# Kernel optimization log

Hardware: AMD Instinct MI355X
Metric: run time of the kernel (lower is better)

Reference implementation:

```python
import jax, jax.numpy as jnp
import numpy as np

TAU = 2.0      # spikingjelly LIFNode default tau
V_TH = 1.0     # default v_threshold
ALPHA = 4.0    # default surrogate.Sigmoid alpha
H, HL = 8, 2   # num_heads, local_heads

@jax.custom_vjp
def spike(u):
    # Heaviside: fire when membrane potential >= threshold (u = v - v_th)
    return (u >= 0.0).astype(u.dtype)

def _spike_fwd(u):
    return spike(u), u

def _spike_bwd(u, g):
    s = jax.nn.sigmoid(ALPHA * u)
    return (g * ALPHA * s * (1.0 - s),)

spike.defvjp(_spike_fwd, _spike_bwd)

def lif(x):
    # Multi-step LIF, decay_input=False, v_reset=0.0 (hard reset), detach_reset=True.
    # Charge: v = v - (v - 0)/tau + x ; spike when v >= v_th ; reset v -> 0 where spiked.
    decay = 1.0 - 1.0 / TAU
    def step(v, xt):
        v = v * decay + xt
        s = spike(v - V_TH)
        v = v * (1.0 - jax.lax.stop_gradient(s))  # detach_reset
        return v, s
    _, spikes = jax.lax.scan(step, jnp.zeros_like(x[0]), x)
    return spikes

def setup_inputs() -> dict:
    key = jax.random.key(0)
    ks = jax.random.split(key, 5)
    T, B, C, D = 4, 8, 512, 768
    hd = D // H            # 96
    mkv = hd * HL          # 192 (GQA kv projection width)
    scale = 0.1            # keeps LIF membrane potentials near threshold
    return {
        "x": jax.random.normal(ks[0], (T, B, C, D), jnp.float32),
        "q_w": jax.random.normal(ks[1], (D, D), jnp.float32) * scale,
        "k_w": jax.random.normal(ks[2], (mkv, D), jnp.float32) * scale,
        "v_w": jax.random.normal(ks[3], (mkv, D), jnp.float32) * scale,
        "wo_w": jax.random.normal(ks[4], (D, D), jnp.float32) * scale,
    }

def reference(x, q_w, k_w, v_w, wo_w):
    T, B, C, D = x.shape
    hd = D // H
    n_rep = H // HL
    xs = lif(x)  # proj_lif
    # q: (T,B,C,D) -> (T,B,H,C,hd)
    q = lif(xs @ q_w.T).reshape(T, B, C, H, hd).transpose(0, 1, 3, 2, 4)
    # k,v: (T,B,C,mkv) -> repeat_interleave over kv heads -> (T,B,H,C,hd)
    k = lif(xs @ k_w.T).reshape(T, B, C, HL, hd)
    k = jnp.repeat(k, n_rep, axis=3).transpose(0, 1, 3, 2, 4)
    v = lif(xs @ v_w.T).reshape(T, B, C, HL, hd)
    v = jnp.repeat(v, n_rep, axis=3).transpose(0, 1, 3, 2, 4)
    # softmax-free attention: (q k^T) * 0.1 @ v
    scores = jnp.einsum('tbhqd,tbhkd->tbhqk', q, k) * 0.1
    out = jnp.einsum('tbhqk,tbhkd->tbhqd', scores, v)
    # (T,B,H,C,hd) -> (T,B,C,D)
    out = out.transpose(0, 1, 3, 2, 4).reshape(T, B, C, D)
    return out @ wo_w.T
```

## Files before the change

kernel.cpp:

```cpp
#include <hip/hip_runtime.h>

typedef __bf16 bf16;
typedef __bf16 bf16x8 __attribute__((ext_vector_type(8)));
typedef float f32x4 __attribute__((ext_vector_type(4)));

#define T_ 4
#define B_ 8
#define C_ 512
#define D_ 768
#define H_ 8
#define HL_ 2
#define HD_ 96
#define MKV_ 192
#define M2_ 4096
#define BCD_ 3145728
#define M3_ 16384
#define NCOMB 1152
#define SUSP_CAP 65536
#define SUSP_WIN 2e-4f

__device__ __forceinline__ void gld16(const bf16* g, bf16* l) {
    __builtin_amdgcn_global_load_lds(
        (const __attribute__((address_space(1))) unsigned int*)g,
        (__attribute__((address_space(3))) unsigned int*)l, 16, 0, 0);
}

__global__ __launch_bounds__(256) void prep_kernel(
    const float* __restrict__ x, const float* __restrict__ q_w,
    const float* __restrict__ k_w, const float* __restrict__ v_w,
    const float* __restrict__ wo_w, bf16* __restrict__ xs,
    bf16* __restrict__ whi, bf16* __restrict__ wlo, bf16* __restrict__ wo_bf,
    unsigned* __restrict__ susp)
{
    const int t0 = blockIdx.x * 256 + threadIdx.x;
    const int stride = gridDim.x * 256;
    if (t0 == 0) susp[0] = 0;
    for (int i = t0; i < BCD_; i += stride) {
        double v = 0.0;
        #pragma unroll
        for (int t = 0; t < T_; ++t) {
            v = v * 0.5 + (double)x[(size_t)t * BCD_ + i];
            float s = (v >= 1.0) ? 1.0f : 0.0f;
            xs[(size_t)t * BCD_ + i] = (bf16)s;
            if (s != 0.0f) v = 0.0;
        }
    }
    for (int i = t0; i < NCOMB * D_; i += stride) {
        int row = i / D_, col = i - row * D_;
        float v;
        if (row < 768)      v = q_w[(size_t)row * D_ + col];
        else if (row < 960) v = k_w[(size_t)(row - 768) * D_ + col];
        else                v = v_w[(size_t)(row - 960) * D_ + col];
        bf16 h = (bf16)v;
        whi[i] = h;
        wlo[i] = (bf16)(v - (float)h);
    }
    for (int i = t0; i < D_ * D_; i += stride)
        wo_bf[i] = (bf16)wo_w[i];
}

__global__ __launch_bounds__(256, 3) void proj_lif_kernel(
    const bf16* __restrict__ xs, const bf16* __restrict__ Whi,
    const bf16* __restrict__ Wlo,
    bf16* __restrict__ q_sp, bf16* __restrict__ k_sp, bf16* __restrict__ v_sp,
    unsigned* __restrict__ susp)
{
    __shared__ __align__(16) bf16 A0[T_][64 * 32];
    __shared__ __align__(16) bf16 A1[T_][64 * 32];
    __shared__ __align__(16) bf16 H0[64 * 32];
    __shared__ __align__(16) bf16 H1[64 * 32];
    __shared__ __align__(16) bf16 L0[64 * 32];
    __shared__ __align__(16) bf16 L1[64 * 32];

    const int tid  = threadIdx.x;
    const int wave = tid >> 6, lane = tid & 63;
    const int m16  = lane & 15, quad = lane >> 4;
    const int wm   = wave >> 1, wn = wave & 1;

    const int bid   = blockIdx.y * 64 + blockIdx.x;
    const int xcd   = bid & 7;
    const int local = bid >> 3;
    const int m0    = ((xcd << 3) | (local & 7)) * 64;
    const int n0    = (local >> 3) * 64;

    const int colb = n0 + wn * 32;
    bf16* outp; int Nloc, cb;
    if (colb < 768)      { outp = q_sp; Nloc = 768; cb = colb; }
    else if (colb < 960) { outp = k_sp; Nloc = 192; cb = colb - 768; }
    else                 { outp = v_sp; Nloc = 192; cb = colb - 960; }

    f32x4 acc[T_][2][2];
    #pragma unroll
    for (int t = 0; t < T_; t++)
        #pragma unroll
        for (int a = 0; a < 2; a++)
            #pragma unroll
            for (int b = 0; b < 2; b++) { f32x4 z = {0.f,0.f,0.f,0.f}; acc[t][a][b] = z; }

    const int srow = tid >> 2;
    const int sseg = (tid & 3) ^ ((tid >> 3) & 3);

#define STAGE(Ab, Hb, Lb, k0) do {                                            \
    _Pragma("unroll")                                                         \
    for (int t = 0; t < T_; t++)                                              \
        gld16(xs + (size_t)(t * M2_ + m0 + srow) * D_ + (k0) + sseg * 8,      \
              &Ab[t][tid * 8]);                                               \
    gld16(Whi + (size_t)(n0 + srow) * D_ + (k0) + sseg * 8, &Hb[tid * 8]);    \
    gld16(Wlo + (size_t)(n0 + srow) * D_ + (k0) + sseg * 8, &Lb[tid * 8]);    \
} while (0)

    bf16x8 a[T_][2], bh[2], bl[2];

#define LOADREGS(Ab, Hb, Lb) do {                                             \
    _Pragma("unroll")                                                         \
    for (int mi = 0; mi < 2; mi++) {                                          \
        int row = wm * 32 + mi * 16 + m16;                                    \
        int off = row * 32 + ((quad ^ ((row >> 1) & 3)) * 8);                 \
        _Pragma("unroll")                                                     \
        for (int t = 0; t < T_; t++) a[t][mi] = *(const bf16x8*)&Ab[t][off];  \
    }                                                                         \
    _Pragma("unroll")                                                         \
    for (int ni = 0; ni < 2; ni++) {                                          \
        int row = wn * 32 + ni * 16 + m16;                                    \
        int off = row * 32 + ((quad ^ ((row >> 1) & 3)) * 8);                 \
        bh[ni] = *(const bf16x8*)&Hb[off];                                    \
        bl[ni] = *(const bf16x8*)&Lb[off];                                    \
    }                                                                         \
} while (0)

#define DOMFMA() do {                                                         \
    __builtin_amdgcn_s_setprio(1);                                            \
    _Pragma("unroll")                                                         \
    for (int ni = 0; ni < 2; ni++)                                            \
        _Pragma("unroll")                                                     \
        for (int t = 0; t < T_; t++)                                          \
            _Pragma("unroll")                                                 \
            for (int mi = 0; mi < 2; mi++) {                                  \
                acc[t][mi][ni] = __builtin_amdgcn_mfma_f32_16x16x32_bf16(     \
                    a[t][mi], bh[ni], acc[t][mi][ni], 0, 0, 0);               \
                acc[t][mi][ni] = __builtin_amdgcn_mfma_f32_16x16x32_bf16(     \
                    a[t][mi], bl[ni], acc[t][mi][ni], 0, 0, 0);               \
            }                                                                 \
    __builtin_amdgcn_s_setprio(0);                                            \
} while (0)

#define READS_DONE() do {                                                     \
    asm volatile("s_waitcnt lgkmcnt(0)" ::: "memory");                        \
    __builtin_amdgcn_s_barrier();                                             \
    __builtin_amdgcn_sched_barrier(0);                                        \
} while (0)

#define NEXT_READY(N) do {                                                    \
    asm volatile("s_waitcnt vmcnt(" #N ")" ::: "memory");                     \
    __builtin_amdgcn_s_barrier();                                             \
} while (0)

    STAGE(A0, H0, L0, 0);
    STAGE(A1, H1, L1, 32);
    NEXT_READY(6);

    for (int s = 0; s < 22; s += 2) {
        LOADREGS(A0, H0, L0);
        READS_DONE();
        STAGE(A0, H0, L0, (s + 2) * 32);
        DOMFMA();
        NEXT_READY(6);

        LOADREGS(A1, H1, L1);
        READS_DONE();
        STAGE(A1, H1, L1, (s + 3) * 32);
        DOMFMA();
        NEXT_READY(6);
    }
    LOADREGS(A0, H0, L0);
    READS_DONE();
    DOMFMA();
    NEXT_READY(0);
    LOADREGS(A1, H1, L1);
    DOMFMA();

#undef STAGE
#undef LOADREGS
#undef DOMFMA
#undef READS_DONE
#undef NEXT_READY

    #pragma unroll
    for (int mi = 0; mi < 2; mi++)
        #pragma unroll
        for (int ni = 0; ni < 2; ni++)
            #pragma unroll
            for (int rr = 0; rr < 4; rr++) {
                int row = m0 + wm * 32 + mi * 16 + quad * 4 + rr;
                int lc  = cb + ni * 16 + m16;
                float v = 0.f;
                bool suspect = false;
                #pragma unroll
                for (int t = 0; t < T_; t++) {
                    v = v * 0.5f + acc[t][mi][ni][rr];
                    float d = v - 1.0f;
                    if (fabsf(d) < SUSP_WIN) suspect = true;
                    float sp = (d >= 0.f) ? 1.f : 0.f;
                    v *= (1.f - sp);
                    outp[(size_t)(t * M2_ + row) * Nloc + lc] = (bf16)sp;
                }
                if (suspect) {
                    int ccol = n0 + wn * 32 + ni * 16 + m16;
                    unsigned idx = atomicAdd(susp, 1u);
                    if (idx < SUSP_CAP) susp[1 + idx] = (unsigned)(row * 2048 + ccol);
                }
            }
}

__global__ __launch_bounds__(256) void fixup_kernel(
    const bf16* __restrict__ xs, const float* __restrict__ q_w,
    const float* __restrict__ k_w, const float* __restrict__ v_w,
    bf16* __restrict__ q_sp, bf16* __restrict__ k_sp, bf16* __restrict__ v_sp,
    const unsigned* __restrict__ susp)
{
    unsigned count = susp[0];
    if (count > SUSP_CAP) count = SUSP_CAP;
    const int lane = threadIdx.x & 63;
    const int wid  = (blockIdx.x * blockDim.x + threadIdx.x) >> 6;
    const int nw   = (gridDim.x * blockDim.x) >> 6;
    for (unsigned i = wid; i < count; i += nw) {
        unsigned e = susp[1 + i];
        int row = e >> 11, col = e & 2047;
        const float* W; bf16* outp; int Nloc, lc;
        if (col < 768)      { W = q_w + (size_t)col * D_;         outp = q_sp; Nloc = 768; lc = col; }
        else if (col < 960) { W = k_w + (size_t)(col - 768) * D_; outp = k_sp; Nloc = 192; lc = col - 768; }
        else                { W = v_w + (size_t)(col - 960) * D_; outp = v_sp; Nloc = 192; lc = col - 960; }
        double v = 0.0;
        for (int t = 0; t < T_; ++t) {
            const bf16* ar = xs + (size_t)(t * M2_ + row) * D_;
            double y = 0.0;
            for (int k = lane; k < D_; k += 64)
                y += (double)(float)ar[k] * (double)W[k];
            #pragma unroll
            for (int off = 1; off < 64; off <<= 1)
                y += __shfl_xor(y, off);
            v = v * 0.5 + y;
            unsigned sp = (v >= 1.0) ? 1u : 0u;
            if (lane == 0) outp[(size_t)(t * M2_ + row) * Nloc + lc] = (bf16)(float)sp;
            if (sp) v = 0.0;
        }
    }
}

__global__ __launch_bounds__(256) void ktv_kernel(
    const bf16* __restrict__ k_sp, const bf16* __restrict__ v_sp,
    float* __restrict__ M_part)
{
    const int g    = blockIdx.x;
    const int cc   = blockIdx.y;
    const int kvh  = g % HL_;
    const int tb   = g / HL_;
    const int wave = threadIdx.x >> 6;
    const int lane = threadIdx.x & 63;
    const int m16  = lane & 15, quad = lane >> 4;

    __shared__ __align__(16) bf16 klds[96 * 40];
    __shared__ __align__(16) bf16 vlds[96 * 40];

    f32x4 acc[9];
    #pragma unroll
    for (int i = 0; i < 9; i++) { f32x4 z = {0.f,0.f,0.f,0.f}; acc[i] = z; }

    const bf16* kbase = k_sp + ((size_t)tb * C_ + cc * 64) * MKV_ + kvh * HD_;
    const bf16* vbase = v_sp + ((size_t)tb * C_ + cc * 64) * MKV_ + kvh * HD_;

    for (int c0 = 0; c0 < 64; c0 += 32) {
        __syncthreads();
        for (int ci = threadIdx.x; ci < 768; ci += 256) {
            int arr = ci & 1;
            int pos = ci >> 1;
            int c = pos / 12, seg = pos - c * 12;
            const bf16* src = (arr ? vbase : kbase) + (size_t)(c0 + c) * MKV_ + seg * 8;
            bf16x8 val = *(const bf16x8*)src;
            bf16* dst = arr ? vlds : klds;
            #pragma unroll
            for (int e = 0; e < 8; e++)
                dst[(seg * 8 + e) * 40 + c] = val[e];
        }
        __syncthreads();
        #pragma unroll
        for (int i = 0; i < 9; i++) {
            int tile = wave + i * 4;
            int mt = tile / 6, nt = tile % 6;
            bf16x8 a = *(const bf16x8*)(&klds[(mt * 16 + m16) * 40 + quad * 8]);
            bf16x8 b = *(const bf16x8*)(&vlds[(nt * 16 + m16) * 40 + quad * 8]);
            acc[i] = __builtin_amdgcn_mfma_f32_16x16x32_bf16(a, b, acc[i], 0, 0, 0);
        }
    }
    float* op = M_part + ((size_t)cc * 64 + g) * HD_ * HD_;
    #pragma unroll
    for (int i = 0; i < 9; i++) {
        int tile = wave + i * 4;
        int mt = tile / 6, nt = tile % 6;
        #pragma unroll
        for (int r = 0; r < 4; r++) {
            int d = mt * 16 + quad * 4 + r;
            int j = nt * 16 + m16;
            op[(size_t)j * HD_ + d] = acc[i][r];
        }
    }
}

__global__ __launch_bounds__(256) void cvtM_kernel(
    const float* __restrict__ M_part, bf16* __restrict__ M_hi,
    bf16* __restrict__ M_lo)
{
    int i = blockIdx.x * 256 + threadIdx.x;
    if (i >= 64 * HD_ * HD_) return;
    float m = 0.f;
    #pragma unroll
    for (int j = 0; j < 8; j++)
        m += M_part[i + (size_t)j * 589824];
    bf16 h = (bf16)m;
    M_hi[i] = h;
    M_lo[i] = (bf16)(m - (float)h);
}

__global__ __launch_bounds__(256) void qm_kernel(
    const bf16* __restrict__ q_sp, const bf16* __restrict__ M_hi,
    const bf16* __restrict__ M_lo, bf16* __restrict__ out_attn)
{
    const int tbh  = blockIdx.x;
    const int h    = tbh % H_;
    const int tb   = tbh / H_;
    const int g    = tb * HL_ + (h >> 2);
    const int wave = threadIdx.x >> 6;
    const int lane = threadIdx.x & 63;
    const int m16  = lane & 15, quad = lane >> 4;
    const int cw   = blockIdx.y * 128 + wave * 32;

    __shared__ __align__(16) bf16 Mh[96 * 104];
    __shared__ __align__(16) bf16 Ml[96 * 104];
    {
        const bf16* gh = M_hi + (size_t)g * HD_ * HD_;
        const bf16* gl = M_lo + (size_t)g * HD_ * HD_;
        #pragma unroll
        for (int j = 0; j < 5; j++) {
            int ci = j * 256 + threadIdx.x;
            if (ci < 1152) {
                int row = ci / 12, seg = ci % 12;
                *(bf16x8*)&Mh[row * 104 + seg * 8] = *(const bf16x8*)(gh + row * HD_ + seg * 8);
                *(bf16x8*)&Ml[row * 104 + seg * 8] = *(const bf16x8*)(gl + row * HD_ + seg * 8);
            }
        }
    }
    __syncthreads();

    f32x4 acc[2][6];
    #pragma unroll
    for (int mi = 0; mi < 2; mi++)
        #pragma unroll
        for (int nt = 0; nt < 6; nt++) { f32x4 z = {0.f,0.f,0.f,0.f}; acc[mi][nt] = z; }

    #pragma unroll
    for (int ks = 0; ks < 3; ++ks) {
        bf16x8 a[2];
        #pragma unroll
        for (int mi = 0; mi < 2; mi++)
            a[mi] = *(const bf16x8*)(q_sp + ((size_t)(tb * C_ + cw + mi * 16 + m16)) * D_
                                     + h * HD_ + ks * 32 + quad * 8);
        #pragma unroll
        for (int nt = 0; nt < 6; ++nt) {
            bf16x8 bh = *(const bf16x8*)&Mh[(nt * 16 + m16) * 104 + ks * 32 + quad * 8];
            bf16x8 bl = *(const bf16x8*)&Ml[(nt * 16 + m16) * 104 + ks * 32 + quad * 8];
            #pragma unroll
            for (int mi = 0; mi < 2; mi++) {
                acc[mi][nt] = __builtin_amdgcn_mfma_f32_16x16x32_bf16(a[mi], bh, acc[mi][nt], 0, 0, 0);
                acc[mi][nt] = __builtin_amdgcn_mfma_f32_16x16x32_bf16(a[mi], bl, acc[mi][nt], 0, 0, 0);
            }
        }
    }
    #pragma unroll
    for (int mi = 0; mi < 2; mi++)
        #pragma unroll
        for (int nt = 0; nt < 6; nt++)
            #pragma unroll
            for (int r = 0; r < 4; r++) {
                int c = cw + mi * 16 + quad * 4 + r;
                int j = nt * 16 + m16;
                out_attn[((size_t)(tb * C_ + c)) * D_ + h * HD_ + j] = (bf16)(0.1f * acc[mi][nt][r]);
            }
}

__global__ __launch_bounds__(256) void final_gemm_kernel(
    const bf16* __restrict__ A, const bf16* __restrict__ W, float* __restrict__ out)
{
    __shared__ __align__(16) bf16 Alds[128 * 64];
    __shared__ __align__(16) bf16 Blds[128 * 64];
    const int tid  = threadIdx.x;
    const int wave = tid >> 6, lane = tid & 63;
    const int m16  = lane & 15, quad = lane >> 4;
    const int wm   = wave >> 1, wn = wave & 1;
    const int m0   = blockIdx.x * 128, n0 = blockIdx.y * 128;

    f32x4 acc[4][4];
    #pragma unroll
    for (int a = 0; a < 4; a++)
        #pragma unroll
        for (int b = 0; b < 4; b++) { f32x4 z = {0.f,0.f,0.f,0.f}; acc[a][b] = z; }

    for (int k0 = 0; k0 < D_; k0 += 64) {
        __syncthreads();
        #pragma unroll
        for (int j = 0; j < 4; j++) {
            int ci = j * 256 + tid;
            int row = ci >> 3, slot = ci & 7;
            int seg = slot ^ ((row >> 1) & 7);
            gld16(A + (size_t)(m0 + row) * D_ + k0 + seg * 8, Alds + ci * 8);
            gld16(W + (size_t)(n0 + row) * D_ + k0 + seg * 8, Blds + ci * 8);
        }
        __syncthreads();
        #pragma unroll
        for (int kc = 0; kc < 2; kc++) {
            bf16x8 a[4], b[4];
            #pragma unroll
            for (int mi = 0; mi < 4; mi++) {
                int row = wm * 64 + mi * 16 + m16;
                a[mi] = *(const bf16x8*)&Alds[row * 64 + (((kc * 4 + quad) ^ ((row >> 1) & 7)) * 8)];
            }
            #pragma unroll
            for (int ni = 0; ni < 4; ni++) {
                int row = wn * 64 + ni * 16 + m16;
                b[ni] = *(const bf16x8*)&Blds[row * 64 + (((kc * 4 + quad) ^ ((row >> 1) & 7)) * 8)];
            }
            #pragma unroll
            for (int mi = 0; mi < 4; mi++)
                #pragma unroll
                for (int ni = 0; ni < 4; ni++)
                    acc[mi][ni] = __builtin_amdgcn_mfma_f32_16x16x32_bf16(a[mi], b[ni], acc[mi][ni], 0, 0, 0);
        }
    }
    #pragma unroll
    for (int mi = 0; mi < 4; mi++)
        #pragma unroll
        for (int ni = 0; ni < 4; ni++)
            #pragma unroll
            for (int r = 0; r < 4; r++) {
                int row = m0 + wm * 64 + mi * 16 + quad * 4 + r;
                int col = n0 + wn * 64 + ni * 16 + m16;
                out[(size_t)row * D_ + col] = acc[mi][ni][r];
            }
}

extern "C" void kernel_launch(void* const* d_in, const int* in_sizes, int n_in,
                              void* d_out, int out_size, void* d_ws, size_t ws_size,
                              hipStream_t stream) {
    const float* x    = (const float*)d_in[0];
    const float* q_w  = (const float*)d_in[1];
    const float* k_w  = (const float*)d_in[2];
    const float* v_w  = (const float*)d_in[3];
    const float* wo_w = (const float*)d_in[4];
    float* out = (float*)d_out;

    char* ws = (char*)d_ws;
    bf16* xs    = (bf16*)(ws);
    bf16* q_sp  = (bf16*)(ws + 25165824);
    bf16* k_sp  = (bf16*)(ws + 50331648);
    bf16* v_sp  = (bf16*)(ws + 56623104);
    bf16* whi   = (bf16*)(ws + 62914560);
    bf16* wlo   = (bf16*)(ws + 64684032);
    bf16* wo_bf = (bf16*)(ws + 66453504);
    bf16* M_hi  = (bf16*)(ws + 67633152);
    bf16* M_lo  = (bf16*)(ws + 68812800);
    unsigned* susp = (unsigned*)(ws + 69992448);
    bf16* out_attn = xs;
    float* M_part  = out;

    hipLaunchKernelGGL(prep_kernel, dim3(2048), dim3(256), 0, stream,
                       x, q_w, k_w, v_w, wo_w, xs, whi, wlo, wo_bf, susp);
    hipLaunchKernelGGL(proj_lif_kernel, dim3(M2_ / 64, NCOMB / 64), dim3(256), 0, stream,
                       xs, whi, wlo, q_sp, k_sp, v_sp, susp);
    hipLaunchKernelGGL(fixup_kernel, dim3(256), dim3(256), 0, stream,
                       xs, q_w, k_w, v_w, q_sp, k_sp, v_sp, susp);
    hipLaunchKernelGGL(ktv_kernel, dim3(T_ * B_ * HL_, 8), dim3(256), 0, stream,
                       k_sp, v_sp, M_part);
    hipLaunchKernelGGL(cvtM_kernel, dim3((64 * HD_ * HD_ + 255) / 256), dim3(256), 0, stream,
                       M_part, M_hi, M_lo);
    hipLaunchKernelGGL(qm_kernel, dim3(T_ * B_ * H_, C_ / 128), dim3(256), 0, stream,
                       q_sp, M_hi, M_lo, out_attn);
    hipLaunchKernelGGL(final_gemm_kernel, dim3(M3_ / 128, D_ / 128), dim3(256), 0, stream,
                       out_attn, wo_bf, out);
}
```

Baseline: 266.0 us.

## Switch spike projection GEMM to int8 MFMA with two-level weight quantization

Spikes are stored as int8 instead of bf16, and the combined q/k/v weights are quantized to two int8 levels (coarse plus residual) using a global max scale. The projection GEMM then uses i8 MFMA with K=64 per instruction, which halves the k-loop iterations and the bytes moved per tile. The larger quantization error is absorbed by widening the suspect window, which sends more elements to the exact fixup kernel; that kernel now adds weights selected by the spike bits instead of multiplying. The cost is an extra max-reduction pass and kernel launch plus a heavier fixup workload.

```diff
diff --git a/kernel.cpp b/kernel.cpp
--- a/kernel.cpp
+++ b/kernel.cpp
@@ -3,6 +3,8 @@
 typedef __bf16 bf16;
 typedef __bf16 bf16x8 __attribute__((ext_vector_type(8)));
 typedef float f32x4 __attribute__((ext_vector_type(4)));
+typedef int i32x4 __attribute__((ext_vector_type(4)));
+typedef signed char i8;
 
 #define T_ 4
 #define B_ 8
@@ -17,19 +19,18 @@
 #define M3_ 16384
 #define NCOMB 1152
 #define SUSP_CAP 65536
-#define SUSP_WIN 2e-4f
-
-__device__ __forceinline__ void gld16(const bf16* g, bf16* l) {
+#define SUSP_WIN 2.2e-3f
+
+__device__ __forceinline__ void gld16(const void* g, void* l) {
     __builtin_amdgcn_global_load_lds(
         (const __attribute__((address_space(1))) unsigned int*)g,
         (__attribute__((address_space(3))) unsigned int*)l, 16, 0, 0);
 }
 
-__global__ __launch_bounds__(256) void prep_kernel(
+__global__ __launch_bounds__(256) void prep_scan_kernel(
     const float* __restrict__ x, const float* __restrict__ q_w,
     const float* __restrict__ k_w, const float* __restrict__ v_w,
-    const float* __restrict__ wo_w, bf16* __restrict__ xs,
-    bf16* __restrict__ whi, bf16* __restrict__ wlo, bf16* __restrict__ wo_bf,
+    i8* __restrict__ xs, unsigned* __restrict__ wmaxb,
     unsigned* __restrict__ susp)
 {
     const int t0 = blockIdx.x * 256 + threadIdx.x;
@@ -40,37 +41,68 @@
         #pragma unroll
         for (int t = 0; t < T_; ++t) {
             v = v * 0.5 + (double)x[(size_t)t * BCD_ + i];
-            float s = (v >= 1.0) ? 1.0f : 0.0f;
-            xs[(size_t)t * BCD_ + i] = (bf16)s;
-            if (s != 0.0f) v = 0.0;
-        }
-    }
+            i8 s = (v >= 1.0) ? (i8)1 : (i8)0;
+            xs[(size_t)t * BCD_ + i] = s;
+            if (s) v = 0.0;
+        }
+    }
+    float m = 0.f;
     for (int i = t0; i < NCOMB * D_; i += stride) {
         int row = i / D_, col = i - row * D_;
         float v;
         if (row < 768)      v = q_w[(size_t)row * D_ + col];
         else if (row < 960) v = k_w[(size_t)(row - 768) * D_ + col];
         else                v = v_w[(size_t)(row - 960) * D_ + col];
-        bf16 h = (bf16)v;
-        whi[i] = h;
-        wlo[i] = (bf16)(v - (float)h);
+        m = fmaxf(m, fabsf(v));
+    }
+    #pragma unroll
+    for (int off = 1; off < 64; off <<= 1)
+        m = fmaxf(m, __shfl_xor(m, off));
+    if ((threadIdx.x & 63) == 0)
+        atomicMax(wmaxb, __float_as_uint(m));
+}
+
+__global__ __launch_bounds__(256) void prep_quant_kernel(
+    const float* __restrict__ q_w, const float* __restrict__ k_w,
+    const float* __restrict__ v_w, const float* __restrict__ wo_w,
+    const unsigned* __restrict__ wmaxb,
+    i8* __restrict__ w1, i8* __restrict__ w2, bf16* __restrict__ wo_bf)
+{
+    const float wmax = __uint_as_float(*wmaxb);
+    const float s1   = wmax * (1.0f / 127.0f);
+    const float s2   = s1 * (1.0f / 127.0f);
+    const float i1   = 1.0f / s1;
+    const float i2   = 1.0f / s2;
+    const int t0 = blockIdx.x * 256 + threadIdx.x;
+    const int stride = gridDim.x * 256;
+    for (int i = t0; i < NCOMB * D_; i += stride) {
+        int row = i / D_, col = i - row * D_;
+        float v;
+        if (row < 768)      v = q_w[(size_t)row * D_ + col];
+        else if (row < 960) v = k_w[(size_t)(row - 768) * D_ + col];
+        else                v = v_w[(size_t)(row - 960) * D_ + col];
+        float h1 = rintf(v * i1);
+        float r  = fmaf(-s1, h1, v);
+        float h2 = rintf(r * i2);
+        w1[i] = (i8)(int)h1;
+        w2[i] = (i8)(int)h2;
     }
     for (int i = t0; i < D_ * D_; i += stride)
         wo_bf[i] = (bf16)wo_w[i];
 }
 
 __global__ __launch_bounds__(256, 3) void proj_lif_kernel(
-    const bf16* __restrict__ xs, const bf16* __restrict__ Whi,
-    const bf16* __restrict__ Wlo,
+    const i8* __restrict__ xs, const i8* __restrict__ W1,
+    const i8* __restrict__ W2, const unsigned* __restrict__ wmaxb,
     bf16* __restrict__ q_sp, bf16* __restrict__ k_sp, bf16* __restrict__ v_sp,
     unsigned* __restrict__ susp)
 {
-    __shared__ __align__(16) bf16 A0[T_][64 * 32];
-    __shared__ __align__(16) bf16 A1[T_][64 * 32];
-    __shared__ __align__(16) bf16 H0[64 * 32];
-    __shared__ __align__(16) bf16 H1[64 * 32];
-    __shared__ __align__(16) bf16 L0[64 * 32];
-    __shared__ __align__(16) bf16 L1[64 * 32];
+    __shared__ __align__(16) i8 A0[T_][64 * 64];
+    __shared__ __align__(16) i8 A1[T_][64 * 64];
+    __shared__ __align__(16) i8 G0[64 * 64];
+    __shared__ __align__(16) i8 G1[64 * 64];
+    __shared__ __align__(16) i8 E0[64 * 64];
+    __shared__ __align__(16) i8 E1[64 * 64];
 
     const int tid  = threadIdx.x;
     const int wave = tid >> 6, lane = tid & 63;
@@ -89,58 +121,62 @@
     else if (colb < 960) { outp = k_sp; Nloc = 192; cb = colb - 768; }
     else                 { outp = v_sp; Nloc = 192; cb = colb - 960; }
 
-    f32x4 acc[T_][2][2];
+    const float s2 = __uint_as_float(*wmaxb) * (1.0f / (127.0f * 127.0f));
+
+    i32x4 acc[T_][2][2];
     #pragma unroll
     for (int t = 0; t < T_; t++)
         #pragma unroll
         for (int a = 0; a < 2; a++)
             #pragma unroll
-            for (int b = 0; b < 2; b++) { f32x4 z = {0.f,0.f,0.f,0.f}; acc[t][a][b] = z; }
+            for (int b = 0; b < 2; b++) { i32x4 z = {0,0,0,0}; acc[t][a][b] = z; }
 
     const int srow = tid >> 2;
     const int sseg = (tid & 3) ^ ((tid >> 3) & 3);
 
-#define STAGE(Ab, Hb, Lb, k0) do {                                            \
+#define STAGE(Ab, Gb, Eb, k0) do {                                            \
     _Pragma("unroll")                                                         \
     for (int t = 0; t < T_; t++)                                              \
-        gld16(xs + (size_t)(t * M2_ + m0 + srow) * D_ + (k0) + sseg * 8,      \
-              &Ab[t][tid * 8]);                                               \
-    gld16(Whi + (size_t)(n0 + srow) * D_ + (k0) + sseg * 8, &Hb[tid * 8]);    \
-    gld16(Wlo + (size_t)(n0 + srow) * D_ + (k0) + sseg * 8, &Lb[tid * 8]);    \
+        gld16(xs + (size_t)(t * M2_ + m0 + srow) * D_ + (k0) + sseg * 16,     \
+              &Ab[t][tid * 16]);                                              \
+    gld16(W1 + (size_t)(n0 + srow) * D_ + (k0) + sseg * 16, &Gb[tid * 16]);   \
+    gld16(W2 + (size_t)(n0 + srow) * D_ + (k0) + sseg * 16, &Eb[tid * 16]);   \
 } while (0)
 
-    bf16x8 a[T_][2], bh[2], bl[2];
-
-#define LOADREGS(Ab, Hb, Lb) do {                                             \
+    i32x4 a[T_][2], b1[2], b2[2];
+
+#define LOADREGS(Ab, Gb, Eb) do {                                             \
     _Pragma("unroll")                                                         \
     for (int mi = 0; mi < 2; mi++) {                                          \
         int row = wm * 32 + mi * 16 + m16;                                    \
-        int off = row * 32 + ((quad ^ ((row >> 1) & 3)) * 8);                 \
+        int off = row * 64 + ((quad ^ ((row >> 1) & 3)) * 16);                \
         _Pragma("unroll")                                                     \
-        for (int t = 0; t < T_; t++) a[t][mi] = *(const bf16x8*)&Ab[t][off];  \
+        for (int t = 0; t < T_; t++) a[t][mi] = *(const i32x4*)&Ab[t][off];   \
     }                                                                         \
     _Pragma("unroll")                                                         \
     for (int ni = 0; ni < 2; ni++) {                                          \
         int row = wn * 32 + ni * 16 + m16;                                    \
-        int off = row * 32 + ((quad ^ ((row >> 1) & 3)) * 8);                 \
-        bh[ni] = *(const bf16x8*)&Hb[off];                                    \
-        bl[ni] = *(const bf16x8*)&Lb[off];                                    \
+        int off = row * 64 + ((quad ^ ((row >> 1) & 3)) * 16);                \
+        b1[ni] = *(const i32x4*)&Gb[off];                                     \
+        b2[ni] = *(const i32x4*)&Eb[off];                                     \
     }                                                                         \
 } while (0)
 
 #define DOMFMA() do {                                                         \
     __builtin_amdgcn_s_setprio(1);                                            \
     _Pragma("unroll")                                                         \
-    for (int ni = 0; ni < 2; ni++)                                            \
+    for (int t = 0; t < T_; t++)                                              \
         _Pragma("unroll")                                                     \
-        for (int t = 0; t < T_; t++)                                          \
+        for (int mi = 0; mi < 2; mi++) {                                      \
+            i32x4 a127 = (a[t][mi] << 7) - a[t][mi];                          \
             _Pragma("unroll")                                                 \
-            for (int mi = 0; mi < 2; mi++) {                                  \
-                acc[t][mi][ni] = __builtin_amdgcn_mfma_f32_16x16x32_bf16(     \
-                    a[t][mi], bh[ni], acc[t][mi][ni], 0, 0, 0);               \
-                acc[t][mi][ni] = __builtin_amdgcn_mfma_f32_16x16x32_bf16(     \
-                    a[t][mi], bl[ni], acc[t][mi][ni], 0, 0, 0);               \
+            for (int ni = 0; ni < 2; ni++) {                                  \
+                acc[t][mi][ni] = __builtin_amdgcn_mfma_i32_16x16x64_i8(       \
+                    a127, b1[ni], acc[t][mi][ni], 0, 0, 0);                   \
+                acc[t][mi][ni] = __builtin_amdgcn_mfma_i32_16x16x64_i8(       \
+                    a[t][mi], b2[ni], acc[t][mi][ni], 0, 0, 0);               \
             }                                                                 \
+        }                                                                     \
     __builtin_amdgcn_s_setprio(0);                                            \
 } while (0)
 
@@ -155,28 +191,28 @@
     __builtin_amdgcn_s_barrier();                                             \
 } while (0)
 
-    STAGE(A0, H0, L0, 0);
-    STAGE(A1, H1, L1, 32);
+    STAGE(A0, G0, E0, 0);
+    STAGE(A1, G1, E1, 64);
     NEXT_READY(6);
 
-    for (int s = 0; s < 22; s += 2) {
-        LOADREGS(A0, H0, L0);
+    for (int s = 0; s < 10; s += 2) {
+        LOADREGS(A0, G0, E0);
         READS_DONE();
-        STAGE(A0, H0, L0, (s + 2) * 32);
+        STAGE(A0, G0, E0, (s + 2) * 64);
         DOMFMA();
         NEXT_READY(6);
 
-        LOADREGS(A1, H1, L1);
+        LOADREGS(A1, G1, E1);
         READS_DONE();
-        STAGE(A1, H1, L1, (s + 3) * 32);
+        STAGE(A1, G1, E1, (s + 3) * 64);
         DOMFMA();
         NEXT_READY(6);
     }
-    LOADREGS(A0, H0, L0);
+    LOADREGS(A0, G0, E0);
     READS_DONE();
     DOMFMA();
     NEXT_READY(0);
-    LOADREGS(A1, H1, L1);
+    LOADREGS(A1, G1, E1);
     DOMFMA();
 
 #undef STAGE
@@ -197,7 +233,7 @@
                 bool suspect = false;
                 #pragma unroll
                 for (int t = 0; t < T_; t++) {
-                    v = v * 0.5f + acc[t][mi][ni][rr];
+                    v = v * 0.5f + s2 * (float)acc[t][mi][ni][rr];
                     float d = v - 1.0f;
                     if (fabsf(d) < SUSP_WIN) suspect = true;
                     float sp = (d >= 0.f) ? 1.f : 0.f;
@@ -213,7 +249,7 @@
 }
 
 __global__ __launch_bounds__(256) void fixup_kernel(
-    const bf16* __restrict__ xs, const float* __restrict__ q_w,
+    const i8* __restrict__ xs, const float* __restrict__ q_w,
     const float* __restrict__ k_w, const float* __restrict__ v_w,
     bf16* __restrict__ q_sp, bf16* __restrict__ k_sp, bf16* __restrict__ v_sp,
     const unsigned* __restrict__ susp)
@@ -232,10 +268,16 @@
         else                { W = v_w + (size_t)(col - 960) * D_; outp = v_sp; Nloc = 192; lc = col - 960; }
         double v = 0.0;
         for (int t = 0; t < T_; ++t) {
-            const bf16* ar = xs + (size_t)(t * M2_ + row) * D_;
+            const i8* ar = xs + (size_t)(t * M2_ + row) * D_;
             double y = 0.0;
-            for (int k = lane; k < D_; k += 64)
-                y += (double)(float)ar[k] * (double)W[k];
+            for (int k = lane * 4; k < D_; k += 256) {
+                f32x4 wv = *(const f32x4*)(W + k);
+                unsigned ab = *(const unsigned*)(ar + k);
+                if (ab & 0x000000ffu) y += (double)wv[0];
+                if (ab & 0x0000ff00u) y += (double)wv[1];
+                if (ab & 0x00ff0000u) y += (double)wv[2];
+                if (ab & 0xff000000u) y += (double)wv[3];
+            }
             #pragma unroll
             for (int off = 1; off < 64; off <<= 1)
                 y += __shfl_xor(y, off);
@@ -458,24 +500,28 @@
     float* out = (float*)d_out;
 
     char* ws = (char*)d_ws;
-    bf16* xs    = (bf16*)(ws);
+    i8*   xs    = (i8*)(ws);
     bf16* q_sp  = (bf16*)(ws + 25165824);
     bf16* k_sp  = (bf16*)(ws + 50331648);
     bf16* v_sp  = (bf16*)(ws + 56623104);
-    bf16* whi   = (bf16*)(ws + 62914560);
-    bf16* wlo   = (bf16*)(ws + 64684032);
+    i8*   w1    = (i8*)(ws + 62914560);
+    i8*   w2    = (i8*)(ws + 63799296);
+    unsigned* wmaxb = (unsigned*)(ws + 64684032);
     bf16* wo_bf = (bf16*)(ws + 66453504);
     bf16* M_hi  = (bf16*)(ws + 67633152);
     bf16* M_lo  = (bf16*)(ws + 68812800);
     unsigned* susp = (unsigned*)(ws + 69992448);
-    bf16* out_attn = xs;
+    bf16* out_attn = (bf16*)ws;
     float* M_part  = out;
 
-    hipLaunchKernelGGL(prep_kernel, dim3(2048), dim3(256), 0, stream,
-                       x, q_w, k_w, v_w, wo_w, xs, whi, wlo, wo_bf, susp);
+    hipMemsetAsync(wmaxb, 0, 4, stream);
+    hipLaunchKernelGGL(prep_scan_kernel, dim3(2048), dim3(256), 0, stream,
+                       x, q_w, k_w, v_w, xs, wmaxb, susp);
+    hipLaunchKernelGGL(prep_quant_kernel, dim3(512), dim3(256), 0, stream,
+                       q_w, k_w, v_w, wo_w, wmaxb, w1, w2, wo_bf);
     hipLaunchKernelGGL(proj_lif_kernel, dim3(M2_ / 64, NCOMB / 64), dim3(256), 0, stream,
-                       xs, whi, wlo, q_sp, k_sp, v_sp, susp);
-    hipLaunchKernelGGL(fixup_kernel, dim3(256), dim3(256), 0, stream,
+                       xs, w1, w2, wmaxb, q_sp, k_sp, v_sp, susp);
+    hipLaunchKernelGGL(fixup_kernel, dim3(512), dim3(256), 0, stream,
                        xs, q_w, k_w, v_w, q_sp, k_sp, v_sp, susp);
     hipLaunchKernelGGL(ktv_kernel, dim3(T_ * B_ * HL_, 8), dim3(256), 0, stream,
                        k_sp, v_sp, M_part);
```

After: 519.0 us. 1.95x slower.

## Load A operand directly into registers in projection GEMM, keep only weights in LDS

Applied to the files above, without the earlier changes.

The projection+LIF kernel no longer stages the spike-input (A) tiles through shared memory. Each wave now owns 16 rows and all 64 columns, and it prefetches its A fragments for all four timesteps straight from global memory into registers, double-buffered across k-steps. Only the hi/lo weight tiles still go through LDS. This cuts LDS footprint and LDS read traffic, and the launch-bounds occupancy hint drops from 3 to 2 blocks per SM. In exchange there are uncoalesced 16-byte global loads per lane, more register pressure, and each weight fragment is now read by all four waves instead of two.

```diff
diff --git a/kernel.cpp b/kernel.cpp
--- a/kernel.cpp
+++ b/kernel.cpp
@@ -59,14 +59,12 @@
         wo_bf[i] = (bf16)wo_w[i];
 }
 
-__global__ __launch_bounds__(256, 3) void proj_lif_kernel(
+__global__ __launch_bounds__(256, 2) void proj_lif_kernel(
     const bf16* __restrict__ xs, const bf16* __restrict__ Whi,
     const bf16* __restrict__ Wlo,
     bf16* __restrict__ q_sp, bf16* __restrict__ k_sp, bf16* __restrict__ v_sp,
     unsigned* __restrict__ susp)
 {
-    __shared__ __align__(16) bf16 A0[T_][64 * 32];
-    __shared__ __align__(16) bf16 A1[T_][64 * 32];
     __shared__ __align__(16) bf16 H0[64 * 32];
     __shared__ __align__(16) bf16 H1[64 * 32];
     __shared__ __align__(16) bf16 L0[64 * 32];
@@ -75,7 +73,6 @@
     const int tid  = threadIdx.x;
     const int wave = tid >> 6, lane = tid & 63;
     const int m16  = lane & 15, quad = lane >> 4;
-    const int wm   = wave >> 1, wn = wave & 1;
 
     const int bid   = blockIdx.y * 64 + blockIdx.x;
     const int xcd   = bid & 7;
@@ -83,64 +80,56 @@
     const int m0    = ((xcd << 3) | (local & 7)) * 64;
     const int n0    = (local >> 3) * 64;
 
-    const int colb = n0 + wn * 32;
     bf16* outp; int Nloc, cb;
-    if (colb < 768)      { outp = q_sp; Nloc = 768; cb = colb; }
-    else if (colb < 960) { outp = k_sp; Nloc = 192; cb = colb - 768; }
-    else                 { outp = v_sp; Nloc = 192; cb = colb - 960; }
-
-    f32x4 acc[T_][2][2];
+    if (n0 < 768)      { outp = q_sp; Nloc = 768; cb = n0; }
+    else if (n0 < 960) { outp = k_sp; Nloc = 192; cb = n0 - 768; }
+    else               { outp = v_sp; Nloc = 192; cb = n0 - 960; }
+
+    f32x4 acc[T_][4];
     #pragma unroll
     for (int t = 0; t < T_; t++)
         #pragma unroll
-        for (int a = 0; a < 2; a++)
-            #pragma unroll
-            for (int b = 0; b < 2; b++) { f32x4 z = {0.f,0.f,0.f,0.f}; acc[t][a][b] = z; }
+        for (int ni = 0; ni < 4; ni++) { f32x4 z = {0.f,0.f,0.f,0.f}; acc[t][ni] = z; }
 
     const int srow = tid >> 2;
     const int sseg = (tid & 3) ^ ((tid >> 3) & 3);
 
-#define STAGE(Ab, Hb, Lb, k0) do {                                            \
+    const bf16* abase = xs + (size_t)(m0 + wave * 16 + m16) * D_ + quad * 8;
+
+#define STAGE_B(Hb, Lb, k0) do {                                              \
+    gld16(Whi + (size_t)(n0 + srow) * D_ + (k0) + sseg * 8, &Hb[tid * 8]);    \
+    gld16(Wlo + (size_t)(n0 + srow) * D_ + (k0) + sseg * 8, &Lb[tid * 8]);    \
+} while (0)
+
+    bf16x8 aP[T_], aN[T_], b1[4], b2[4];
+
+#define PREF_A(dst, k0) do {                                                  \
     _Pragma("unroll")                                                         \
     for (int t = 0; t < T_; t++)                                              \
-        gld16(xs + (size_t)(t * M2_ + m0 + srow) * D_ + (k0) + sseg * 8,      \
-              &Ab[t][tid * 8]);                                               \
-    gld16(Whi + (size_t)(n0 + srow) * D_ + (k0) + sseg * 8, &Hb[tid * 8]);    \
-    gld16(Wlo + (size_t)(n0 + srow) * D_ + (k0) + sseg * 8, &Lb[tid * 8]);    \
-} while (0)
-
-    bf16x8 a[T_][2], bh[2], bl[2];
-
-#define LOADREGS(Ab, Hb, Lb) do {                                             \
+        dst[t] = *(const bf16x8*)(abase + (size_t)t * (size_t)(M2_) * D_ + (k0)); \
+} while (0)
+
+#define LOADREGS_B(Hb, Lb) do {                                               \
     _Pragma("unroll")                                                         \
-    for (int mi = 0; mi < 2; mi++) {                                          \
-        int row = wm * 32 + mi * 16 + m16;                                    \
+    for (int ni = 0; ni < 4; ni++) {                                          \
+        int row = ni * 16 + m16;                                              \
         int off = row * 32 + ((quad ^ ((row >> 1) & 3)) * 8);                 \
-        _Pragma("unroll")                                                     \
-        for (int t = 0; t < T_; t++) a[t][mi] = *(const bf16x8*)&Ab[t][off];  \
+        b1[ni] = *(const bf16x8*)&Hb[off];                                    \
+        b2[ni] = *(const bf16x8*)&Lb[off];                                    \
     }                                                                         \
-    _Pragma("unroll")                                                         \
-    for (int ni = 0; ni < 2; ni++) {                                          \
-        int row = wn * 32 + ni * 16 + m16;                                    \
-        int off = row * 32 + ((quad ^ ((row >> 1) & 3)) * 8);                 \
-        bh[ni] = *(const bf16x8*)&Hb[off];                                    \
-        bl[ni] = *(const bf16x8*)&Lb[off];                                    \
-    }                                                                         \
-} while (0)
-
-#define DOMFMA() do {                                                         \
+} while (0)
+
+#define DOMFMA(av) do {                                                       \
     __builtin_amdgcn_s_setprio(1);                                            \
     _Pragma("unroll")                                                         \
-    for (int ni = 0; ni < 2; ni++)                                            \
+    for (int t = 0; t < T_; t++)                                              \
         _Pragma("unroll")                                                     \
-        for (int t = 0; t < T_; t++)                                          \
-            _Pragma("unroll")                                                 \
-            for (int mi = 0; mi < 2; mi++) {                                  \
-                acc[t][mi][ni] = __builtin_amdgcn_mfma_f32_16x16x32_bf16(     \
-                    a[t][mi], bh[ni], acc[t][mi][ni], 0, 0, 0);               \
-                acc[t][mi][ni] = __builtin_amdgcn_mfma_f32_16x16x32_bf16(     \
-                    a[t][mi], bl[ni], acc[t][mi][ni], 0, 0, 0);               \
-            }                                                                 \
+        for (int ni = 0; ni < 4; ni++) {                                      \
+            acc[t][ni] = __builtin_amdgcn_mfma_f32_16x16x32_bf16(             \
+                av[t], b1[ni], acc[t][ni], 0, 0, 0);                          \
+            acc[t][ni] = __builtin_amdgcn_mfma_f32_16x16x32_bf16(             \
+                av[t], b2[ni], acc[t][ni], 0, 0, 0);                          \
+        }                                                                     \
     __builtin_amdgcn_s_setprio(0);                                            \
 } while (0)
 
@@ -155,61 +144,67 @@
     __builtin_amdgcn_s_barrier();                                             \
 } while (0)
 
-    STAGE(A0, H0, L0, 0);
-    STAGE(A1, H1, L1, 32);
+    STAGE_B(H0, L0, 0);
+    STAGE_B(H1, L1, 32);
+    __builtin_amdgcn_sched_barrier(0);
+    PREF_A(aP, 0);
     NEXT_READY(6);
 
     for (int s = 0; s < 22; s += 2) {
-        LOADREGS(A0, H0, L0);
+        LOADREGS_B(H0, L0);
         READS_DONE();
-        STAGE(A0, H0, L0, (s + 2) * 32);
-        DOMFMA();
+        STAGE_B(H0, L0, (s + 2) * 32);
+        __builtin_amdgcn_sched_barrier(0);
+        PREF_A(aN, (s + 1) * 32);
+        DOMFMA(aP);
         NEXT_READY(6);
 
-        LOADREGS(A1, H1, L1);
+        LOADREGS_B(H1, L1);
         READS_DONE();
-        STAGE(A1, H1, L1, (s + 3) * 32);
-        DOMFMA();
+        STAGE_B(H1, L1, (s + 3) * 32);
+        __builtin_amdgcn_sched_barrier(0);
+        PREF_A(aP, (s + 2) * 32);
+        DOMFMA(aN);
         NEXT_READY(6);
     }
-    LOADREGS(A0, H0, L0);
+    LOADREGS_B(H0, L0);
     READS_DONE();
-    DOMFMA();
-    NEXT_READY(0);
-    LOADREGS(A1, H1, L1);
-    DOMFMA();
-
-#undef STAGE
-#undef LOADREGS
+    PREF_A(aN, 23 * 32);
+    DOMFMA(aP);
+    NEXT_READY(4);
+    LOADREGS_B(H1, L1);
+    DOMFMA(aN);
+
+#undef STAGE_B
+#undef PREF_A
+#undef LOADREGS_B
 #undef DOMFMA
 #undef READS_DONE
 #undef NEXT_READY
 
     #pragma unroll
-    for (int mi = 0; mi < 2; mi++)
-        #pragma unroll
-        for (int ni = 0; ni < 2; ni++)
-            #pragma unroll
-            for (int rr = 0; rr < 4; rr++) {
-                int row = m0 + wm * 32 + mi * 16 + quad * 4 + rr;
-                int lc  = cb + ni * 16 + m16;
-                float v = 0.f;
-                bool suspect = false;
-                #pragma unroll
-                for (int t = 0; t < T_; t++) {
-                    v = v * 0.5f + acc[t][mi][ni][rr];
-                    float d = v - 1.0f;
-                    if (fabsf(d) < SUSP_WIN) suspect = true;
-                    float sp = (d >= 0.f) ? 1.f : 0.f;
-                    v *= (1.f - sp);
-                    outp[(size_t)(t * M2_ + row) * Nloc + lc] = (bf16)sp;
-                }
-                if (suspect) {
-                    int ccol = n0 + wn * 32 + ni * 16 + m16;
-                    unsigned idx = atomicAdd(susp, 1u);
-                    if (idx < SUSP_CAP) susp[1 + idx] = (unsigned)(row * 2048 + ccol);
-                }
-            }
+    for (int ni = 0; ni < 4; ni++)
+        #pragma unroll
+        for (int rr = 0; rr < 4; rr++) {
+            int row = m0 + wave * 16 + quad * 4 + rr;
+            int lc  = cb + ni * 16 + m16;
+            float v = 0.f;
+            bool suspect = false;
+            #pragma unroll
+            for (int t = 0; t < T_; t++) {
+                v = v * 0.5f + acc[t][ni][rr];
+                float d = v - 1.0f;
+                if (fabsf(d) < SUSP_WIN) suspect = true;
+                float sp = (d >= 0.f) ? 1.f : 0.f;
+                v *= (1.f - sp);
+                outp[(size_t)(t * M2_ + row) * Nloc + lc] = (bf16)sp;
+            }
+            if (suspect) {
+                int ccol = n0 + ni * 16 + m16;
+                unsigned idx = atomicAdd(susp, 1u);
+                if (idx < SUSP_CAP) susp[1 + idx] = (unsigned)(row * 2048 + ccol);
+            }
+        }
 }
 
 __global__ __launch_bounds__(256) void fixup_kernel(
```

After: 278.6 us. 4.8% more time.
